# Kernel tuning notes

Hardware: AMD Instinct MI355X
Metric: run time of the kernel (lower is better)

The kernel has to match this reference:

```python
import jax, jax.numpy as jnp
import numpy as np

N_NODES = 50000
N_EDGES = 800000
N_IN = 256
N_H = 64


def _xavier(key, fan_in, fan_out):
    limit = np.sqrt(6.0 / (fan_in + fan_out)).astype(np.float32)
    return jax.random.uniform(key, (fan_in, fan_out), jnp.float32, -limit, limit)


def setup_inputs() -> dict:
    key = jax.random.key(0)
    ks = jax.random.split(key, 12)
    inp = {
        "bf": jax.random.normal(ks[0], (1, N_NODES, N_IN), jnp.float32),
        "bl": jax.random.normal(ks[1], (1, N_NODES, N_IN), jnp.float32),
        "shuf_fts": jax.random.normal(ks[2], (1, N_NODES, N_IN), jnp.float32),
        "shuf_fls": jax.random.normal(ks[3], (1, N_NODES, N_IN), jnp.float32),
        "adj_rows": jax.random.randint(ks[4], (N_EDGES,), 0, N_NODES, jnp.int32),
        "adj_cols": jax.random.randint(ks[5], (N_EDGES,), 0, N_NODES, jnp.int32),
        "adj_w": jax.random.uniform(ks[6], (N_EDGES,), jnp.float32),
        "diff_rows": jax.random.randint(ks[7], (N_EDGES,), 0, N_NODES, jnp.int32),
        "diff_cols": jax.random.randint(ks[8], (N_EDGES,), 0, N_NODES, jnp.int32),
        "diff_w": jax.random.uniform(ks[9], (N_EDGES,), jnp.float32),
        # GCN parameters (Linear has bias=False; separate additive bias init 0; PReLU slope 0.25)
        "W1": _xavier(ks[10], N_IN, N_H),
        "b1": jnp.zeros((N_H,), jnp.float32),
        "a1": jnp.float32(0.25),
        "W2": _xavier(ks[11], N_IN, N_H),
        "b2": jnp.zeros((N_H,), jnp.float32),
        "a2": jnp.float32(0.25),
    }
    return inp


def _gcn(seq, W, b, a, rows, cols, w):
    # seq: [1, N, F_in]; sparse spmm: out[r] = sum_e 1[rows[e]==r] * w[e] * fts[cols[e]]
    fts = seq[0] @ W                                   # [N, n_h]
    msgs = w[:, None] * fts[cols]                      # [E, n_h] gather
    agg = jax.ops.segment_sum(msgs, rows, num_segments=N_NODES)  # [N, n_h] scatter-add
    out = agg[None, :, :] + b                          # bias add
    return jnp.where(out >= 0, out, a * out)           # PReLU


def reference(bf, bl, shuf_fts, shuf_fls, adj_rows, adj_cols, adj_w,
              diff_rows, diff_cols, diff_w, W1, b1, a1, W2, b2, a2):
    h_1 = _gcn(bf, W1, b1, a1, adj_rows, adj_cols, adj_w)
    h_2 = _gcn(bl, W2, b2, a2, diff_rows, diff_cols, diff_w)
    h_3 = _gcn(shuf_fts, W1, b1, a1, adj_rows, adj_cols, adj_w)
    h_4 = _gcn(shuf_fls, W2, b2, a2, diff_rows, diff_cols, diff_w)
    return jnp.stack([h_1, h_2, h_3, h_4])             # [4, 1, N, n_h]
```

## Files before the change

kernel.cpp:

```cpp
#include <hip/hip_runtime.h>
#include <hip/hip_bf16.h>

#define N_NODES 50000
#define N_EDGES 800000
#define N_IN    256
#define N_H     64
#define NB      125
#define RPB     400
#define BCAP    8192
#define EPT     8
#define BIN_BLK 2048

typedef short short8 __attribute__((ext_vector_type(8)));
typedef float f32x4  __attribute__((ext_vector_type(4)));

__device__ inline short f2bf(float f) {
    __bf16 h = (__bf16)f;
    return (short)__builtin_bit_cast(unsigned short, h);
}
__device__ inline float bflo(unsigned int q) { return __uint_as_float(q << 16); }
__device__ inline float bfhi(unsigned int q) { return __uint_as_float(q & 0xFFFF0000u); }


__global__ __launch_bounds__(256) void k_bin(
    const int* __restrict__ adj_rows, const int* __restrict__ adj_cols,
    const float* __restrict__ adj_w,
    const int* __restrict__ diff_rows, const int* __restrict__ diff_cols,
    const float* __restrict__ diff_w,
    int* __restrict__ gcnt, int2* __restrict__ bin) {

    int g = blockIdx.y;
    const int*   rows = g ? diff_rows : adj_rows;
    const int*   cols = g ? diff_cols : adj_cols;
    const float* ww   = g ? diff_w    : adj_w;
    int base_e = blockIdx.x * BIN_BLK;
    int t = threadIdx.x;

    __shared__ int lcnt[NB];
    __shared__ int lbase[NB];
    for (int i = t; i < NB; i += 256) lcnt[i] = 0;
    __syncthreads();

    int lpos[EPT];
    int bkt[EPT];
    #pragma unroll
    for (int e = 0; e < EPT; ++e) {
        int idx = base_e + e * 256 + t;
        if (idx < N_EDGES) {
            int r = rows[idx];
            int b = r / RPB;
            bkt[e] = b;
            lpos[e] = atomicAdd(&lcnt[b], 1);
        } else bkt[e] = -1;
    }
    __syncthreads();
    for (int i = t; i < NB; i += 256) lbase[i] = atomicAdd(&gcnt[g * NB + i], lcnt[i]);
    __syncthreads();

    #pragma unroll
    for (int e = 0; e < EPT; ++e) {
        int idx = base_e + e * 256 + t;
        if (idx < N_EDGES) {
            unsigned int r = (unsigned int)rows[idx];
            unsigned int c = (unsigned int)cols[idx];
            int b = bkt[e];
            int2 m;
            m.x = (int)((r << 16) | c);
            m.y = __float_as_int(ww[idx]);
            bin[((size_t)(g * NB + b)) * BCAP + lbase[b] + lpos[e]] = m;
        }
    }
}


__global__ __launch_bounds__(256) void k_build(
    const int* __restrict__ gcnt, const int2* __restrict__ bin,
    int2* __restrict__ csr, int* __restrict__ row_ptr) {

    int g = blockIdx.y, b = blockIdx.x, t = threadIdx.x;
    __shared__ int hist[512];
    __shared__ int s2[256];
    __shared__ int sbase;

    for (int i = t; i < 512; i += 256) hist[i] = 0;
    __syncthreads();

    int cnt = gcnt[g * NB + b];
    const int2* be = bin + ((size_t)(g * NB + b)) * BCAP;
    int r0 = b * RPB;

    for (int i = t; i < cnt; i += 256) {
        unsigned int rc = (unsigned int)be[i].x;
        atomicAdd(&hist[(rc >> 16) - r0], 1);
    }
    __syncthreads();

    if (t == 0) {
        int s = 0;
        for (int i = 0; i < b; ++i) s += gcnt[g * NB + i];
        sbase = s;
    }

    int v0 = hist[2 * t], v1 = hist[2 * t + 1];
    int local = v0 + v1;
    s2[t] = local;
    __syncthreads();
    for (int off = 1; off < 256; off <<= 1) {
        int v = (t >= off) ? s2[t - off] : 0;
        __syncthreads();
        s2[t] += v;
        __syncthreads();
    }
    int e0 = sbase + (s2[t] - local);
    int e1 = e0 + v0;

    int* rp = row_ptr + g * (N_NODES + 1);
    if (2 * t < RPB)     rp[r0 + 2 * t]     = e0;
    if (2 * t + 1 < RPB) rp[r0 + 2 * t + 1] = e1;
    __syncthreads();
    hist[2 * t] = e0;
    hist[2 * t + 1] = e1;
    __syncthreads();

    int2* cg = csr + (size_t)g * N_EDGES;
    for (int i = t; i < cnt; i += 256) {
        int2 m = be[i];
        unsigned int rc = (unsigned int)m.x;
        int lr = (int)(rc >> 16) - r0;
        int pos = atomicAdd(&hist[lr], 1);
        int2 o;
        o.x = (int)(rc & 0xFFFFu);
        o.y = m.y;
        cg[pos] = o;
    }
    if (b == NB - 1 && t == 0) rp[N_NODES] = N_EDGES;
}


__global__ __launch_bounds__(256) void k_gemm(
    const float* __restrict__ X0, const float* __restrict__ X1,
    const float* __restrict__ X2, const float* __restrict__ X3,
    const float* __restrict__ W1, const float* __restrict__ W2,
    unsigned short* __restrict__ Tadj, unsigned short* __restrict__ Tdiff) {

    const float* X; const float* W; unsigned short* T; int coloff;
    switch (blockIdx.y) {
        case 0:  X = X0; W = W1; T = Tadj;  coloff = 0;  break;
        case 1:  X = X2; W = W1; T = Tadj;  coloff = 64; break;
        case 2:  X = X1; W = W2; T = Tdiff; coloff = 0;  break;
        default: X = X3; W = W2; T = Tdiff; coloff = 64; break;
    }

    __shared__ __align__(16) unsigned short WT[64][264];
    for (int i = threadIdx.x; i < N_IN * N_H; i += 256) {
        int k = i >> 6, c = i & 63;
        WT[c][k] = (unsigned short)f2bf(W[i]);
    }
    __syncthreads();

    int wid  = threadIdx.x >> 6;
    int lane = threadIdx.x & 63;
    int rb = (blockIdx.x * 4 + wid) * 16;
    if (rb >= N_NODES) return;

    int arow = rb + (lane & 15);
    int kg   = lane >> 4;
    const float* ap = X + (size_t)arow * N_IN + kg * 8;

    f32x4 acc[4];
    for (int ct = 0; ct < 4; ++ct) acc[ct] = (f32x4){0.f, 0.f, 0.f, 0.f};

    for (int kt = 0; kt < 8; ++kt) {
        const float4* p = reinterpret_cast<const float4*>(ap + kt * 32);
        float4 a0 = p[0];
        float4 a1 = p[1];
        short8 af;
        af[0] = f2bf(a0.x); af[1] = f2bf(a0.y); af[2] = f2bf(a0.z); af[3] = f2bf(a0.w);
        af[4] = f2bf(a1.x); af[5] = f2bf(a1.y); af[6] = f2bf(a1.z); af[7] = f2bf(a1.w);
        #pragma unroll
        for (int ct = 0; ct < 4; ++ct) {
            const unsigned short* wp = &WT[ct * 16 + (lane & 15)][kt * 32 + kg * 8];
            short8 bfr = *reinterpret_cast<const short8*>(wp);
            acc[ct] = __builtin_amdgcn_mfma_f32_16x16x32_bf16(af, bfr, acc[ct], 0, 0, 0);
        }
    }

    int rgrp = lane >> 4;
    #pragma unroll
    for (int ct = 0; ct < 4; ++ct) {
        int col = coloff + ct * 16 + (lane & 15);
        #pragma unroll
        for (int r = 0; r < 4; ++r) {
            int row = rb + rgrp * 4 + r;
            T[(size_t)row * 128 + col] = (unsigned short)f2bf(acc[ct][r]);
        }
    }
}


__global__ __launch_bounds__(256) void k_agg(
    const int* __restrict__ row_ptr, const int2* __restrict__ csr,
    const unsigned int* __restrict__ Tadj, const unsigned int* __restrict__ Tdiff,
    const float* __restrict__ b1, const float* __restrict__ a1,
    const float* __restrict__ b2, const float* __restrict__ a2,
    float* __restrict__ out) {

    int wid  = threadIdx.x >> 6;
    int lane = threadIdx.x & 63;
    int node = blockIdx.x * 4 + wid;
    int g    = blockIdx.y;

    const int* rp = row_ptr + g * (N_NODES + 1);
    const int2* el = csr + (size_t)g * N_EDGES;
    const unsigned int* Tu = g ? Tdiff : Tadj;

    int e  = rp[node];
    int e1 = rp[node + 1];
    float ax = 0.f, ay = 0.f;

    for (; e + 4 <= e1; e += 4) {
        int2 m0 = el[e + 0], m1 = el[e + 1], m2 = el[e + 2], m3 = el[e + 3];
        unsigned int q0 = Tu[(size_t)m0.x * 64 + lane];
        unsigned int q1 = Tu[(size_t)m1.x * 64 + lane];
        unsigned int q2 = Tu[(size_t)m2.x * 64 + lane];
        unsigned int q3 = Tu[(size_t)m3.x * 64 + lane];
        float w0 = __int_as_float(m0.y), w1 = __int_as_float(m1.y);
        float w2 = __int_as_float(m2.y), w3 = __int_as_float(m3.y);
        ax += w0 * bflo(q0); ay += w0 * bfhi(q0);
        ax += w1 * bflo(q1); ay += w1 * bfhi(q1);
        ax += w2 * bflo(q2); ay += w2 * bfhi(q2);
        ax += w3 * bflo(q3); ay += w3 * bfhi(q3);
    }
    for (; e < e1; ++e) {
        int2 m = el[e];
        unsigned int q = Tu[(size_t)m.x * 64 + lane];
        float w = __int_as_float(m.y);
        ax += w * bflo(q); ay += w * bfhi(q);
    }

    const float* bias = g ? b2 : b1;
    float slope = g ? a2[0] : a1[0];
    int f = 2 * lane;
    size_t base;
    int fo;
    if (lane < 32) { base = g ? (size_t)3200000 : (size_t)0;       fo = f; }
    else           { base = g ? (size_t)9600000 : (size_t)6400000; fo = f - 64; }
    float v0 = ax + bias[fo];
    float v1 = ay + bias[fo + 1];
    v0 = (v0 >= 0.f) ? v0 : slope * v0;
    v1 = (v1 >= 0.f) ? v1 : slope * v1;
    float2 res; res.x = v0; res.y = v1;
    *reinterpret_cast<float2*>(out + base + (size_t)node * 64 + fo) = res;
}


extern "C" void kernel_launch(void* const* d_in, const int* in_sizes, int n_in,
                              void* d_out, int out_size, void* d_ws, size_t ws_size,
                              hipStream_t stream) {
    const float* bf_      = (const float*)d_in[0];
    const float* bl_      = (const float*)d_in[1];
    const float* shuf_fts = (const float*)d_in[2];
    const float* shuf_fls = (const float*)d_in[3];
    const int*   adj_rows = (const int*)d_in[4];
    const int*   adj_cols = (const int*)d_in[5];
    const float* adj_w    = (const float*)d_in[6];
    const int*   diff_rows= (const int*)d_in[7];
    const int*   diff_cols= (const int*)d_in[8];
    const float* diff_w   = (const float*)d_in[9];
    const float* W1       = (const float*)d_in[10];
    const float* b1       = (const float*)d_in[11];
    const float* a1       = (const float*)d_in[12];
    const float* W2       = (const float*)d_in[13];
    const float* b2       = (const float*)d_in[14];
    const float* a2       = (const float*)d_in[15];
    float* out = (float*)d_out;

    char* ws = (char*)d_ws;
    unsigned short* Tadj  = (unsigned short*)(ws);
    unsigned short* Tdiff = (unsigned short*)(ws + 12800000);
    int2* csr             = (int2*)(ws + 25600000);
    int*  row_ptr         = (int*)(ws + 38400000);
    int*  gcnt            = (int*)(ws + 38801024);

    int2* bin = (int2*)d_out;

    hipMemsetAsync(gcnt, 0, 2 * NB * sizeof(int), stream);

    k_bin<<<dim3((N_EDGES + BIN_BLK - 1) / BIN_BLK, 2), dim3(256), 0, stream>>>(
        adj_rows, adj_cols, adj_w, diff_rows, diff_cols, diff_w, gcnt, bin);
    k_build<<<dim3(NB, 2), dim3(256), 0, stream>>>(gcnt, bin, csr, row_ptr);

    k_gemm<<<dim3((N_NODES + 63) / 64, 4), dim3(256), 0, stream>>>(
        bf_, bl_, shuf_fts, shuf_fls, W1, W2, Tadj, Tdiff);

    k_agg<<<dim3(N_NODES / 4, 2), dim3(256), 0, stream>>>(
        row_ptr, csr, (const unsigned int*)Tadj, (const unsigned int*)Tdiff,
        b1, a1, b2, a2, out);
}
```

Measured before the change: 193.6 us.

## Precompute bf16 transposed weights once and share B fragments across paired inputs

Adds a small kernel that converts W1/W2 to a transposed bf16 layout in workspace once, so GEMM blocks copy it into LDS with vector loads instead of each block converting fp32 weights itself. The GEMM now handles both inputs that share a weight matrix in one wave, reusing each LDS B fragment for two MFMAs, and uses 512-thread blocks covering 128 rows. This cuts repeated weight conversion and LDS traffic per block. In exchange there is an extra launch, higher register pressure from doubled accumulators, and a new row bounds check on the tail.

```diff
diff --git a/kernel.cpp b/kernel.cpp
--- a/kernel.cpp
+++ b/kernel.cpp
@@ -10,6 +10,7 @@
 #define BCAP    8192
 #define EPT     8
 #define BIN_BLK 2048
+#define GSTRIDE 264
 
 typedef short short8 __attribute__((ext_vector_type(8)));
 typedef float f32x4  __attribute__((ext_vector_type(4)));
@@ -137,62 +138,90 @@
 }
 
 
-__global__ __launch_bounds__(256) void k_gemm(
+__global__ __launch_bounds__(256) void k_wt(const float* __restrict__ W1,
+                                            const float* __restrict__ W2,
+                                            unsigned short* __restrict__ WTg) {
+    int g = blockIdx.x;
+    const float* W = g ? W2 : W1;
+    unsigned short* o = WTg + (size_t)g * 64 * GSTRIDE;
+    for (int i = threadIdx.x; i < N_IN * N_H; i += 256) {
+        int k = i >> 6, c = i & 63;
+        o[c * GSTRIDE + k] = (unsigned short)f2bf(W[i]);
+    }
+}
+
+
+__global__ __launch_bounds__(512, 6) void k_gemm(
     const float* __restrict__ X0, const float* __restrict__ X1,
     const float* __restrict__ X2, const float* __restrict__ X3,
-    const float* __restrict__ W1, const float* __restrict__ W2,
+    const unsigned short* __restrict__ WTg,
     unsigned short* __restrict__ Tadj, unsigned short* __restrict__ Tdiff) {
 
-    const float* X; const float* W; unsigned short* T; int coloff;
-    switch (blockIdx.y) {
-        case 0:  X = X0; W = W1; T = Tadj;  coloff = 0;  break;
-        case 1:  X = X2; W = W1; T = Tadj;  coloff = 64; break;
-        case 2:  X = X1; W = W2; T = Tdiff; coloff = 0;  break;
-        default: X = X3; W = W2; T = Tdiff; coloff = 64; break;
-    }
-
-    __shared__ __align__(16) unsigned short WT[64][264];
-    for (int i = threadIdx.x; i < N_IN * N_H; i += 256) {
-        int k = i >> 6, c = i & 63;
-        WT[c][k] = (unsigned short)f2bf(W[i]);
+    int g = blockIdx.y;
+    const float* Xa = g ? X1 : X0;
+    const float* Xb = g ? X3 : X2;
+    unsigned short* T = g ? Tdiff : Tadj;
+    const unsigned short* src = WTg + (size_t)g * 64 * GSTRIDE;
+
+    __shared__ __align__(16) unsigned short WT[64 * GSTRIDE];
+    {
+        const uint4* s4 = (const uint4*)src;
+        uint4* d4 = (uint4*)WT;
+        int t = threadIdx.x;
+        #pragma unroll
+        for (int j = 0; j < 4; ++j) d4[t + 512 * j] = s4[t + 512 * j];
+        if (t < 64) d4[2048 + t] = s4[2048 + t];
     }
     __syncthreads();
 
     int wid  = threadIdx.x >> 6;
     int lane = threadIdx.x & 63;
-    int rb = (blockIdx.x * 4 + wid) * 16;
+    int rb = blockIdx.x * 128 + wid * 16;
     if (rb >= N_NODES) return;
 
     int arow = rb + (lane & 15);
     int kg   = lane >> 4;
-    const float* ap = X + (size_t)arow * N_IN + kg * 8;
-
-    f32x4 acc[4];
-    for (int ct = 0; ct < 4; ++ct) acc[ct] = (f32x4){0.f, 0.f, 0.f, 0.f};
+    const float* apa = Xa + (size_t)arow * N_IN + kg * 8;
+    const float* apb = Xb + (size_t)arow * N_IN + kg * 8;
+
+    f32x4 acc[2][4];
+    #pragma unroll
+    for (int s = 0; s < 2; ++s)
+        #pragma unroll
+        for (int ct = 0; ct < 4; ++ct) acc[s][ct] = (f32x4){0.f, 0.f, 0.f, 0.f};
 
     for (int kt = 0; kt < 8; ++kt) {
-        const float4* p = reinterpret_cast<const float4*>(ap + kt * 32);
-        float4 a0 = p[0];
-        float4 a1 = p[1];
-        short8 af;
-        af[0] = f2bf(a0.x); af[1] = f2bf(a0.y); af[2] = f2bf(a0.z); af[3] = f2bf(a0.w);
-        af[4] = f2bf(a1.x); af[5] = f2bf(a1.y); af[6] = f2bf(a1.z); af[7] = f2bf(a1.w);
+        const float4* pa = reinterpret_cast<const float4*>(apa + kt * 32);
+        const float4* pb = reinterpret_cast<const float4*>(apb + kt * 32);
+        float4 a0 = pa[0];
+        float4 a1 = pa[1];
+        float4 c0 = pb[0];
+        float4 c1 = pb[1];
+        short8 afa, afb;
+        afa[0] = f2bf(a0.x); afa[1] = f2bf(a0.y); afa[2] = f2bf(a0.z); afa[3] = f2bf(a0.w);
+        afa[4] = f2bf(a1.x); afa[5] = f2bf(a1.y); afa[6] = f2bf(a1.z); afa[7] = f2bf(a1.w);
+        afb[0] = f2bf(c0.x); afb[1] = f2bf(c0.y); afb[2] = f2bf(c0.z); afb[3] = f2bf(c0.w);
+        afb[4] = f2bf(c1.x); afb[5] = f2bf(c1.y); afb[6] = f2bf(c1.z); afb[7] = f2bf(c1.w);
         #pragma unroll
         for (int ct = 0; ct < 4; ++ct) {
-            const unsigned short* wp = &WT[ct * 16 + (lane & 15)][kt * 32 + kg * 8];
+            const unsigned short* wp = &WT[(ct * 16 + (lane & 15)) * GSTRIDE + kt * 32 + kg * 8];
             short8 bfr = *reinterpret_cast<const short8*>(wp);
-            acc[ct] = __builtin_amdgcn_mfma_f32_16x16x32_bf16(af, bfr, acc[ct], 0, 0, 0);
+            acc[0][ct] = __builtin_amdgcn_mfma_f32_16x16x32_bf16(afa, bfr, acc[0][ct], 0, 0, 0);
+            acc[1][ct] = __builtin_amdgcn_mfma_f32_16x16x32_bf16(afb, bfr, acc[1][ct], 0, 0, 0);
         }
     }
 
     int rgrp = lane >> 4;
     #pragma unroll
     for (int ct = 0; ct < 4; ++ct) {
-        int col = coloff + ct * 16 + (lane & 15);
+        int col = ct * 16 + (lane & 15);
         #pragma unroll
         for (int r = 0; r < 4; ++r) {
             int row = rb + rgrp * 4 + r;
-            T[(size_t)row * 128 + col] = (unsigned short)f2bf(acc[ct][r]);
+            if (row < N_NODES) {
+                T[(size_t)row * 128 + col]      = (unsigned short)f2bf(acc[0][ct][r]);
+                T[(size_t)row * 128 + 64 + col] = (unsigned short)f2bf(acc[1][ct][r]);
+            }
         }
     }
 }
@@ -281,6 +310,7 @@
     int2* csr             = (int2*)(ws + 25600000);
     int*  row_ptr         = (int*)(ws + 38400000);
     int*  gcnt            = (int*)(ws + 38801024);
+    unsigned short* WTg   = (unsigned short*)(ws + 38803072);
 
     int2* bin = (int2*)d_out;
 
@@ -288,10 +318,11 @@
 
     k_bin<<<dim3((N_EDGES + BIN_BLK - 1) / BIN_BLK, 2), dim3(256), 0, stream>>>(
         adj_rows, adj_cols, adj_w, diff_rows, diff_cols, diff_w, gcnt, bin);
+    k_wt<<<dim3(2), dim3(256), 0, stream>>>(W1, W2, WTg);
     k_build<<<dim3(NB, 2), dim3(256), 0, stream>>>(gcnt, bin, csr, row_ptr);
 
-    k_gemm<<<dim3((N_NODES + 63) / 64, 4), dim3(256), 0, stream>>>(
-        bf_, bl_, shuf_fts, shuf_fls, W1, W2, Tadj, Tdiff);
+    k_gemm<<<dim3((N_NODES + 127) / 128, 2), dim3(512), 0, stream>>>(
+        bf_, bl_, shuf_fts, shuf_fls, WTg, Tadj, Tdiff);
 
     k_agg<<<dim3(N_NODES / 4, 2), dim3(256), 0, stream>>>(
         row_ptr, csr, (const unsigned int*)Tadj, (const unsigned int*)Tdiff,
```

After: 216.7 us. 1.12x slower.
